# Kernel optimization log

Hardware: AMD Instinct MI355X
Metric: run time of the kernel (lower is better)

## Reference

```python
import jax, jax.numpy as jnp
import numpy as np

N, K, D, H = 2048, 128, 768, 512


def setup_inputs() -> dict:
    key = jax.random.key(0)
    k1, k2, k3, k4, k5, k6 = jax.random.split(key, 6)
    image_feat = jax.random.normal(k1, (N, D), dtype=jnp.float32)
    text_feat = jax.random.normal(k2, (K, D), dtype=jnp.float32)
    # nn.Linear(2D, H): weight (H, 2D), bias (H); stored transposed for clean matmul
    W1 = jax.random.normal(k3, (2 * D, H), dtype=jnp.float32) * (1.0 / np.sqrt(2 * D))
    b1 = jax.random.normal(k4, (H,), dtype=jnp.float32) * 0.01
    # nn.Linear(H, 1)
    W2 = jax.random.normal(k5, (H, 1), dtype=jnp.float32) * (1.0 / np.sqrt(H))
    b2 = jax.random.normal(k6, (1,), dtype=jnp.float32) * 0.01
    return {"image_feat": image_feat, "text_feat": text_feat,
            "W1": W1, "b1": b1, "W2": W2, "b2": b2}


def reference(image_feat, text_feat, W1, b1, W2, b2):
    # concat([img, txt]) @ W1 == img @ W1[:D] + txt @ W1[D:]  (same math,
    # avoids materializing the (N,K,2D) concatenated tensor)
    img_proj = image_feat @ W1[:D]          # (N, H)
    txt_proj = text_feat @ W1[D:]           # (K, H)
    h = jax.nn.relu(img_proj[:, None, :] + txt_proj[None, :, :] + b1)  # (N, K, H)
    sim = (h @ W2).squeeze(-1) + b2[0]      # (N, K)
    return sim
```

## Files before the change

kernel.cpp:

```cpp
#include <hip/hip_runtime.h>
#include <hip/hip_bf16.h>

#define N_IMG 2048
#define K_TXT 128
#define D_IN  768
#define H_DIM 512
#define M_TOT (N_IMG + K_TXT)
#define NK    (N_IMG * K_TXT)
#define NTILE 16

typedef __bf16 bf16x8 __attribute__((ext_vector_type(8)));
typedef float  f32x4  __attribute__((ext_vector_type(4)));

__global__ __launch_bounds__(256) void proj_kernel(
    const float* __restrict__ img, const float* __restrict__ txt,
    const float* __restrict__ W1, const float* __restrict__ b1,
    const float* __restrict__ W2, float* __restrict__ P,
    float* __restrict__ pw2)
{
    __shared__ __align__(16) __bf16 As[32][72];
    __shared__ __align__(16) __bf16 Bs[32][72];
    __shared__ float lds_pw[32];

    const int tid = threadIdx.x;
    const int n0 = (blockIdx.x & (NTILE - 1)) * 32;
    const int m0 = (blockIdx.x >> 4) * 32;
    const bool is_txt = (m0 >= N_IMG);
    const float* X  = is_txt ? (txt + (size_t)(m0 - N_IMG) * D_IN)
                             : (img + (size_t)m0 * D_IN);
    const float* Wb = W1 + (is_txt ? (size_t)D_IN * H_DIM : 0);

    const int wave = tid >> 6, lane = tid & 63;
    const int wm = (wave >> 1) * 16, wn = (wave & 1) * 16;
    const int quad = lane >> 4, lm = lane & 15;

    const int ar = tid >> 3, ak = (tid & 7) * 8;
    const int bn = tid & 31, bk = (tid >> 5) * 8;

    f32x4 acc = {0.f, 0.f, 0.f, 0.f};
    f32x4 aR0, aR1;
    float bR[8];

    auto loadA = [&](int kc) {
        const float* ap = X + (size_t)ar * D_IN + kc + ak;
        aR0 = *(const f32x4*)(ap + 0);
        aR1 = *(const f32x4*)(ap + 4);
    };
    auto loadB = [&](int kc) {
        #pragma unroll
        for (int j = 0; j < 8; ++j)
            bR[j] = Wb[(size_t)(kc + bk + j) * H_DIM + n0 + bn];
    };

    union BPack { __bf16 h[8]; uint4 u; };

    loadA(0); loadB(0);

    for (int it = 0; it < 12; ++it) {
        BPack pa;
        #pragma unroll
        for (int j = 0; j < 4; ++j) { pa.h[j] = (__bf16)aR0[j]; pa.h[4+j] = (__bf16)aR1[j]; }
        *(uint4*)&As[ar][ak] = pa.u;
        BPack q;
        #pragma unroll
        for (int j = 0; j < 8; ++j) q.h[j] = (__bf16)bR[j];
        *(uint4*)&Bs[bn][bk] = q.u;
        __syncthreads();

        if (it < 11) { loadA((it + 1) * 64); loadB((it + 1) * 64); }

        #pragma unroll
        for (int sub = 0; sub < 2; ++sub) {
            bf16x8 af = *(bf16x8*)&As[wm + lm][sub * 32 + quad * 8];
            bf16x8 bf = *(bf16x8*)&Bs[wn + lm][sub * 32 + quad * 8];
            acc = __builtin_amdgcn_mfma_f32_16x16x32_bf16(af, bf, acc, 0, 0, 0);
        }
        __syncthreads();
    }

    float rv[4];
    {
        const int gn = n0 + wn + lm;
        const float badd = is_txt ? b1[gn] : 0.0f;
        const float w2h = 0.5f * W2[gn];
        #pragma unroll
        for (int r = 0; r < 4; ++r) {
            const int gm = m0 + wm + quad * 4 + r;
            const float v = acc[r] + badd;
            P[(size_t)gm * H_DIM + gn] = v;
            rv[r] = v * w2h;
        }
    }
    #pragma unroll
    for (int m = 1; m < 16; m <<= 1) {
        #pragma unroll
        for (int r = 0; r < 4; ++r) rv[r] += __shfl_xor(rv[r], m, 64);
    }
    if (tid < 32) lds_pw[tid] = 0.f;
    __syncthreads();
    if (lm == 0) {
        #pragma unroll
        for (int r = 0; r < 4; ++r)
            atomicAdd(&lds_pw[wm + quad * 4 + r], rv[r]);
    }
    __syncthreads();
    if (tid < 32)
        pw2[(size_t)(blockIdx.x & (NTILE - 1)) * M_TOT + m0 + tid] = lds_pw[tid];
}

__global__ __launch_bounds__(256) void sim_kernel(
    const float* __restrict__ P, const float* __restrict__ W2,
    float* __restrict__ P2)
{
    __shared__ __align__(16) float Bs[64][67];
    __shared__ __align__(16) float Ws[64];

    const int tid = threadIdx.x;
    const int n0 = blockIdx.x * 32;
    const int k0 = blockIdx.y * 64;
    const int hs = blockIdx.z;
    const int hc = hs * 64;

    #pragma unroll
    for (int i = 0; i < 4; ++i) {
        const int flat = tid + i * 256;
        const int row = flat >> 4, c4 = flat & 15;
        f32x4 v = *(const f32x4*)(P + (size_t)(N_IMG + k0 + row) * H_DIM + hc + c4 * 4);
        *(f32x4*)&Bs[row][c4 * 4] = v;
    }
    if (tid < 16) {
        f32x4 w = *(const f32x4*)(W2 + hc + tid * 4);
        w *= 0.5f;
        *(f32x4*)&Ws[tid * 4] = w;
    }
    __syncthreads();

    const int tx = tid & 15;
    const int ty = tid >> 4;
    const float* pA = P + (size_t)(n0 + ty * 2) * H_DIM + hc;

    f32x4 acc0 = {0.f, 0.f, 0.f, 0.f};
    f32x4 acc1 = {0.f, 0.f, 0.f, 0.f};

    #pragma unroll 4
    for (int h4 = 0; h4 < 16; ++h4) {
        f32x4 a0 = *(const f32x4*)(pA + h4 * 4);
        f32x4 a1 = *(const f32x4*)(pA + H_DIM + h4 * 4);
        f32x4 w  = *(f32x4*)&Ws[h4 * 4];
        f32x4 b[4];
        #pragma unroll
        for (int j = 0; j < 4; ++j) b[j] = *(f32x4*)&Bs[tx * 4 + j][h4 * 4];

        #pragma unroll
        for (int j = 0; j < 4; ++j) {
            #pragma unroll
            for (int hh = 0; hh < 4; ++hh) {
                const float t0 = a0[hh] + b[j][hh];
                acc0[j] = fmaf(fabsf(t0), w[hh], acc0[j]);
                const float t1 = a1[hh] + b[j][hh];
                acc1[j] = fmaf(fabsf(t1), w[hh], acc1[j]);
            }
        }
    }

    float* o = P2 + (size_t)hs * NK + (size_t)(n0 + ty * 2) * K_TXT + k0 + tx * 4;
    *(f32x4*)o = acc0;
    *(f32x4*)(o + K_TXT) = acc1;
}

__global__ __launch_bounds__(256) void reduce_kernel(
    const float* __restrict__ P2, const float* __restrict__ pw2,
    const float* __restrict__ b2, float* __restrict__ out)
{
    const int idx = blockIdx.x * 256 + threadIdx.x;
    const int n  = idx >> 5;
    const int k4 = (idx & 31) * 4;
    const size_t base = (size_t)n * K_TXT + k4;

    f32x4 s = {0.f, 0.f, 0.f, 0.f};
    #pragma unroll
    for (int hs = 0; hs < 8; ++hs)
        s += *(const f32x4*)(P2 + (size_t)hs * NK + base);

    float pn = 0.f;
    f32x4 pk = {0.f, 0.f, 0.f, 0.f};
    #pragma unroll
    for (int sl = 0; sl < NTILE; ++sl) {
        const float* pws = pw2 + (size_t)sl * M_TOT;
        pn += pws[n];
        pk += *(const f32x4*)(pws + N_IMG + k4);
    }

    const float add = pn + b2[0];
    s[0] += add + pk[0]; s[1] += add + pk[1];
    s[2] += add + pk[2]; s[3] += add + pk[3];
    *(f32x4*)(out + base) = s;
}

extern "C" void kernel_launch(void* const* d_in, const int* in_sizes, int n_in,
                              void* d_out, int out_size, void* d_ws, size_t ws_size,
                              hipStream_t stream) {
    const float* img = (const float*)d_in[0];
    const float* txt = (const float*)d_in[1];
    const float* W1  = (const float*)d_in[2];
    const float* b1  = (const float*)d_in[3];
    const float* W2  = (const float*)d_in[4];
    const float* b2  = (const float*)d_in[5];
    float* out = (float*)d_out;

    float* P   = (float*)d_ws;
    float* pw2 = P + (size_t)M_TOT * H_DIM;
    float* P2  = pw2 + (size_t)NTILE * M_TOT;

    proj_kernel  <<<dim3(68 * NTILE),           256, 0, stream>>>(img, txt, W1, b1, W2, P, pw2);
    sim_kernel   <<<dim3(N_IMG / 32, K_TXT / 64, H_DIM / 64), 256, 0, stream>>>(P, W2, P2);
    reduce_kernel<<<dim3(NK / 4 / 256),         256, 0, stream>>>(P2, pw2, b2, out);
}
```

Measured before the change: 100.6 us.

## Retile sim kernel into four H slabs with swizzled LDS and fewer partials

Splits the hidden dimension into four slabs of 128 instead of eight of 64 and retiles each block as 64 image rows by 32 text rows, with each thread handling 4x2 outputs. The text tile in LDS gets an XOR swizzle to avoid bank conflicts, and W2 is read straight from global memory instead of being staged in LDS. Fewer slabs halve the partial-sum traffic written to P2 and read back in the reduce kernel. The reduce kernel now precomputes the per-row and per-column pw2 sums once per block in shared memory. In exchange, each thread carries a longer loop and issues more global loads of image rows per step.

```diff
diff --git a/kernel.cpp b/kernel.cpp
--- a/kernel.cpp
+++ b/kernel.cpp
@@ -8,9 +8,12 @@
 #define M_TOT (N_IMG + K_TXT)
 #define NK    (N_IMG * K_TXT)
 #define NTILE 16
+#define NSLAB 4
+#define HS    (H_DIM / NSLAB)
 
 typedef __bf16 bf16x8 __attribute__((ext_vector_type(8)));
 typedef float  f32x4  __attribute__((ext_vector_type(4)));
+typedef float  f32x2  __attribute__((ext_vector_type(2)));
 
 __global__ __launch_bounds__(256) void proj_kernel(
     const float* __restrict__ img, const float* __restrict__ txt,
@@ -112,88 +115,103 @@
     const float* __restrict__ P, const float* __restrict__ W2,
     float* __restrict__ P2)
 {
-    __shared__ __align__(16) float Bs[64][67];
-    __shared__ __align__(16) float Ws[64];
+    __shared__ __align__(16) float Bs[32][HS];
 
     const int tid = threadIdx.x;
-    const int n0 = blockIdx.x * 32;
-    const int k0 = blockIdx.y * 64;
+    const int n0 = blockIdx.x * 64;
+    const int k0 = blockIdx.y * 32;
     const int hs = blockIdx.z;
-    const int hc = hs * 64;
+    const int hc = hs * HS;
 
     #pragma unroll
     for (int i = 0; i < 4; ++i) {
         const int flat = tid + i * 256;
-        const int row = flat >> 4, c4 = flat & 15;
+        const int row = flat >> 5, c4 = flat & 31;
         f32x4 v = *(const f32x4*)(P + (size_t)(N_IMG + k0 + row) * H_DIM + hc + c4 * 4);
-        *(f32x4*)&Bs[row][c4 * 4] = v;
-    }
-    if (tid < 16) {
-        f32x4 w = *(const f32x4*)(W2 + hc + tid * 4);
-        w *= 0.5f;
-        *(f32x4*)&Ws[tid * 4] = w;
+        const int sc4 = c4 ^ ((row >> 1) & 7);
+        *(f32x4*)&Bs[row][sc4 * 4] = v;
     }
     __syncthreads();
 
     const int tx = tid & 15;
     const int ty = tid >> 4;
-    const float* pA = P + (size_t)(n0 + ty * 2) * H_DIM + hc;
-
-    f32x4 acc0 = {0.f, 0.f, 0.f, 0.f};
-    f32x4 acc1 = {0.f, 0.f, 0.f, 0.f};
+    const int bswz = tx & 7;
+    const int r0 = tx * 2;
+    const float* pA = P + (size_t)(n0 + ty * 4) * H_DIM + hc;
+
+    f32x2 acc[4];
+    #pragma unroll
+    for (int nn = 0; nn < 4; ++nn) acc[nn] = f32x2{0.f, 0.f};
 
     #pragma unroll 4
-    for (int h4 = 0; h4 < 16; ++h4) {
-        f32x4 a0 = *(const f32x4*)(pA + h4 * 4);
-        f32x4 a1 = *(const f32x4*)(pA + H_DIM + h4 * 4);
-        f32x4 w  = *(f32x4*)&Ws[h4 * 4];
-        f32x4 b[4];
-        #pragma unroll
-        for (int j = 0; j < 4; ++j) b[j] = *(f32x4*)&Bs[tx * 4 + j][h4 * 4];
-
-        #pragma unroll
-        for (int j = 0; j < 4; ++j) {
+    for (int h4 = 0; h4 < HS / 4; ++h4) {
+        const int sc = (h4 ^ bswz) * 4;
+        f32x4 w  = *(const f32x4*)(W2 + hc + h4 * 4);
+        f32x4 b0 = *(f32x4*)&Bs[r0][sc];
+        f32x4 b1 = *(f32x4*)&Bs[r0 + 1][sc];
+        f32x4 a[4];
+        #pragma unroll
+        for (int nn = 0; nn < 4; ++nn)
+            a[nn] = *(const f32x4*)(pA + (size_t)nn * H_DIM + h4 * 4);
+
+        #pragma unroll
+        for (int nn = 0; nn < 4; ++nn) {
             #pragma unroll
             for (int hh = 0; hh < 4; ++hh) {
-                const float t0 = a0[hh] + b[j][hh];
-                acc0[j] = fmaf(fabsf(t0), w[hh], acc0[j]);
-                const float t1 = a1[hh] + b[j][hh];
-                acc1[j] = fmaf(fabsf(t1), w[hh], acc1[j]);
+                const float t0 = a[nn][hh] + b0[hh];
+                acc[nn][0] = fmaf(fabsf(t0), w[hh], acc[nn][0]);
+                const float t1 = a[nn][hh] + b1[hh];
+                acc[nn][1] = fmaf(fabsf(t1), w[hh], acc[nn][1]);
             }
         }
     }
 
-    float* o = P2 + (size_t)hs * NK + (size_t)(n0 + ty * 2) * K_TXT + k0 + tx * 4;
-    *(f32x4*)o = acc0;
-    *(f32x4*)(o + K_TXT) = acc1;
+    float* o = P2 + (size_t)hs * NK + (size_t)(n0 + ty * 4) * K_TXT + k0 + tx * 2;
+    #pragma unroll
+    for (int nn = 0; nn < 4; ++nn) {
+        f32x2 st = { acc[nn][0] * 0.5f, acc[nn][1] * 0.5f };
+        *(f32x2*)(o + (size_t)nn * K_TXT) = st;
+    }
 }
 
 __global__ __launch_bounds__(256) void reduce_kernel(
     const float* __restrict__ P2, const float* __restrict__ pw2,
     const float* __restrict__ b2, float* __restrict__ out)
 {
-    const int idx = blockIdx.x * 256 + threadIdx.x;
-    const int n  = idx >> 5;
-    const int k4 = (idx & 31) * 4;
-    const size_t base = (size_t)n * K_TXT + k4;
+    __shared__ float pn_l[8];
+    __shared__ __align__(16) float pk_l[K_TXT];
+
+    const int tid = threadIdx.x;
+    const int n0 = blockIdx.x * 8;
+
+    if (tid < 8) {
+        float s = 0.f;
+        #pragma unroll
+        for (int sl = 0; sl < NTILE; ++sl)
+            s += pw2[(size_t)sl * M_TOT + n0 + tid];
+        pn_l[tid] = s;
+    } else if (tid >= 128) {
+        const int k = tid - 128;
+        float s = 0.f;
+        #pragma unroll
+        for (int sl = 0; sl < NTILE; ++sl)
+            s += pw2[(size_t)sl * M_TOT + N_IMG + k];
+        pk_l[k] = s;
+    }
+    __syncthreads();
+
+    const int kq = tid & 31, nr = tid >> 5;
+    const size_t base = (size_t)(n0 + nr) * K_TXT + kq * 4;
 
     f32x4 s = {0.f, 0.f, 0.f, 0.f};
     #pragma unroll
-    for (int hs = 0; hs < 8; ++hs)
-        s += *(const f32x4*)(P2 + (size_t)hs * NK + base);
-
-    float pn = 0.f;
-    f32x4 pk = {0.f, 0.f, 0.f, 0.f};
-    #pragma unroll
-    for (int sl = 0; sl < NTILE; ++sl) {
-        const float* pws = pw2 + (size_t)sl * M_TOT;
-        pn += pws[n];
-        pk += *(const f32x4*)(pws + N_IMG + k4);
-    }
-
-    const float add = pn + b2[0];
-    s[0] += add + pk[0]; s[1] += add + pk[1];
-    s[2] += add + pk[2]; s[3] += add + pk[3];
+    for (int sl = 0; sl < NSLAB; ++sl)
+        s += *(const f32x4*)(P2 + (size_t)sl * NK + base);
+
+    const float add = pn_l[nr] + b2[0];
+    f32x4 pk4 = *(f32x4*)&pk_l[kq * 4];
+    s[0] += add + pk4[0]; s[1] += add + pk4[1];
+    s[2] += add + pk4[2]; s[3] += add + pk4[3];
     *(f32x4*)(out + base) = s;
 }
 
@@ -212,7 +230,7 @@
     float* pw2 = P + (size_t)M_TOT * H_DIM;
     float* P2  = pw2 + (size_t)NTILE * M_TOT;
 
-    proj_kernel  <<<dim3(68 * NTILE),           256, 0, stream>>>(img, txt, W1, b1, W2, P, pw2);
-    sim_kernel   <<<dim3(N_IMG / 32, K_TXT / 64, H_DIM / 64), 256, 0, stream>>>(P, W2, P2);
-    reduce_kernel<<<dim3(NK / 4 / 256),         256, 0, stream>>>(P2, pw2, b2, out);
-}
+    proj_kernel  <<<dim3(68 * NTILE),                     256, 0, stream>>>(img, txt, W1, b1, W2, P, pw2);
+    sim_kernel   <<<dim3(N_IMG / 64, K_TXT / 32, NSLAB),  256, 0, stream>>>(P, W2, P2);
+    reduce_kernel<<<dim3(N_IMG / 8),                      256, 0, stream>>>(P2, pw2, b2, out);
+}
```

Result: no change. 100.2 us (-0.3%).
